# Kernel tuning notes

Measured on AMD Instinct MI355X. Metric: run time of the kernel, lower is better.

The kernel has to match this reference:

```python
import jax, jax.numpy as jnp
import numpy as np

N = 100000   # nodes
E = 1600000  # edges (avg degree 16)
H = 8        # heads
C = 64       # per-head channels
G = 64       # graphs in batch
IN = 3       # input channels
OUT = 10     # classes
NEG_SLOPE = 0.2  # PyG GATConv default


def setup_inputs() -> dict:
    key = jax.random.key(0)
    ks = jax.random.split(key, 16)
    s = 0.1
    return {
        "x": jax.random.normal(ks[0], (N, IN), jnp.float32),
        "edge_index": jax.random.randint(ks[1], (2, E), 0, N),
        "batch": jnp.sort(jax.random.randint(ks[2], (N,), 0, G)),
        "W1": jax.random.normal(ks[3], (IN, H * C), jnp.float32) * s,
        "a1s": jax.random.normal(ks[4], (H, C), jnp.float32) * s,
        "a1d": jax.random.normal(ks[5], (H, C), jnp.float32) * s,
        "b1": jnp.zeros((H * C,), jnp.float32),
        "W2": jax.random.normal(ks[6], (H * C, H * C), jnp.float32) * s,
        "a2s": jax.random.normal(ks[7], (H, C), jnp.float32) * s,
        "a2d": jax.random.normal(ks[8], (H, C), jnp.float32) * s,
        "b2": jnp.zeros((H * C,), jnp.float32),
        "Wc": jax.random.normal(ks[9], (H * C, OUT), jnp.float32) * s,
        "bc": jnp.zeros((OUT,), jnp.float32),
    }


def _gat_layer(x, W, a_s, a_d, b, src, dst, n):
    # h: [N, H, C] per-head projected features
    h = (x @ W).reshape(n, H, C)
    # per-node attention logits per head
    al_s = jnp.einsum('nhc,hc->nh', h, a_s)
    al_d = jnp.einsum('nhc,hc->nh', h, a_d)
    # per-edge raw scores, [E', H]
    e = jax.nn.leaky_relu(al_s[src] + al_d[dst], NEG_SLOPE)
    # segment softmax over incoming edges of each destination node
    m = jax.ops.segment_max(e, dst, num_segments=n)
    ex = jnp.exp(e - m[dst])
    den = jax.ops.segment_sum(ex, dst, num_segments=n)
    alpha = ex / den[dst]  # [E', H]
    # weighted scatter-aggregate of source messages
    out = jax.ops.segment_sum(alpha[:, :, None] * h[src], dst, num_segments=n)
    return out.reshape(n, H * C) + b


def reference(x, edge_index, batch, W1, a1s, a1d, b1, W2, a2s, a2d, b2, Wc, bc):
    n = x.shape[0]
    ar = jnp.arange(n)
    # PyG GATConv adds self-loops by default
    src = jnp.concatenate([edge_index[0], ar])
    dst = jnp.concatenate([edge_index[1], ar])

    x1 = jax.nn.elu(_gat_layer(x, W1, a1s, a1d, b1, src, dst, n))
    x2 = jax.nn.elu(_gat_layer(x1, W2, a2s, a2d, b2, src, dst, n))

    # global mean pool over graphs
    sums = jax.ops.segment_sum(x2, batch, num_segments=G)
    cnt = jax.ops.segment_sum(jnp.ones((n, 1), x2.dtype), batch, num_segments=G)
    pooled = sums / jnp.maximum(cnt, 1.0)
    return pooled @ Wc + bc
```

## Files before the change

kernel.cpp:

```cpp
#include <hip/hip_runtime.h>
#include <math.h>

#define N_NODES 100000
#define N_EDGES 1600000
#define EP (N_EDGES + N_NODES)
#define NH 8
#define NC 64
#define NG 64
#define HC 512
#define SCAN_BLOCKS ((N_NODES + 255) / 256)
#define NPART 32
#define BPSTR 80

typedef unsigned short bf16_t;
typedef unsigned char fp8_t;
typedef __attribute__((ext_vector_type(8))) short short8;
typedef __attribute__((ext_vector_type(4))) float floatx4;
typedef __attribute__((ext_vector_type(2))) float floatx2;

__device__ inline bf16_t f2bf(float f) {
    union { float f; unsigned int i; } x;
    x.f = f;
    unsigned int b = x.i;
    return (bf16_t)((b + 0x7fffu + ((b >> 16) & 1u)) >> 16);
}
__device__ inline fp8_t f2fp8(float f) {
    int v = __builtin_amdgcn_cvt_pk_fp8_f32(f, f, 0, false);
    return (fp8_t)v;
}

__device__ inline void ldsload16(const void* g, void* l) {
    __builtin_amdgcn_global_load_lds(
        (const __attribute__((address_space(1))) unsigned int*)g,
        (__attribute__((address_space(3))) unsigned int*)l, 16, 0, 0);
}

#define NBW2T (HC * HC / 256)
__global__ void k_prepw2t(const float* __restrict__ W1, const float* __restrict__ a1s,
                          const float* __restrict__ a1d, float* __restrict__ wprep,
                          const float* __restrict__ W2, bf16_t* __restrict__ W2T) {
    if (blockIdx.x == NBW2T) {
        int t = threadIdx.x;
        if (t < 48) {
            int isD = t >= 24;
            int tt = t % 24;
            int h = tt / 3, k = tt % 3;
            const float* a = isD ? a1d : a1s;
            float s = 0.f;
            for (int c = 0; c < 64; c++) s += W1[k * HC + h * 64 + c] * a[h * 64 + c];
            wprep[t] = s;
        }
        return;
    }
    int i = blockIdx.x * 256 + threadIdx.x;
    int n = i >> 9, kp = i & 511;
    int k = (kp & 7) * 64 + (kp >> 3);
    W2T[i] = f2bf(W2[k * HC + n]);
}

__global__ void k_deg(const int* __restrict__ ei, int* __restrict__ deg) {
    int i = blockIdx.x * 256 + threadIdx.x;
    if (i >= EP) return;
    int d = (i < N_EDGES) ? ei[N_EDGES + i] : (i - N_EDGES);
    atomicAdd(&deg[d], 1);
}

__global__ void k_scan1(const int* __restrict__ deg, int* __restrict__ rowptr, int* __restrict__ part) {
    __shared__ int s[256];
    int t = threadIdx.x, i = blockIdx.x * 256 + t;
    int v = (i < N_NODES) ? deg[i] : 0;
    s[t] = v;
    __syncthreads();
    for (int off = 1; off < 256; off <<= 1) {
        int u = (t >= off) ? s[t - off] : 0;
        __syncthreads();
        s[t] += u;
        __syncthreads();
    }
    if (i < N_NODES) rowptr[i] = s[t] - v;
    if (t == 255) part[blockIdx.x] = s[t];
}

__global__ void k_scan2(int* __restrict__ part, int* __restrict__ rowptr, int* __restrict__ gstart) {
    __shared__ int s[512];
    int t = threadIdx.x;
    int v = (t < SCAN_BLOCKS) ? part[t] : 0;
    s[t] = v;
    __syncthreads();
    for (int off = 1; off < 512; off <<= 1) {
        int u = (t >= off) ? s[t - off] : 0;
        __syncthreads();
        s[t] += u;
        __syncthreads();
    }
    part[t] = s[t] - v;
    if (t == 0) rowptr[N_NODES] = EP;
    if (t <= NG) gstart[t] = N_NODES;
}

__global__ void k_scan3(const int* __restrict__ part, int* __restrict__ rowptr,
                        int* __restrict__ cursor, const float* __restrict__ x,
                        float* __restrict__ xp, const int* __restrict__ batch,
                        int* __restrict__ gstart) {
    int i = blockIdx.x * 256 + threadIdx.x;
    if (i < N_NODES) {
        int v = rowptr[i] + part[blockIdx.x];
        rowptr[i] = v;
        cursor[i] = v;
        xp[i * 4 + 0] = x[i * 3 + 0];
        xp[i * 4 + 1] = x[i * 3 + 1];
        xp[i * 4 + 2] = x[i * 3 + 2];
        xp[i * 4 + 3] = 0.f;
        int b = batch[i];
        if (i == 0) {
            for (int g = 0; g <= b; g++) gstart[g] = 0;
        } else {
            int bp = batch[i - 1];
            if (b != bp)
                for (int g = bp + 1; g <= b; g++) gstart[g] = i;
        }
    }
}

__global__ void k_scatter(const int* __restrict__ ei, int* __restrict__ cursor, int* __restrict__ csr) {
    int i = blockIdx.x * 256 + threadIdx.x;
    if (i >= EP) return;
    int s, d;
    if (i < N_EDGES) { s = ei[i]; d = ei[N_EDGES + i]; }
    else { s = i - N_EDGES; d = s; }
    int pos = atomicAdd(&cursor[d], 1);
    csr[pos] = s;
}

__global__ __launch_bounds__(256) void k_layer1(
    const float* __restrict__ xp, const int* __restrict__ rowptr, const int* __restrict__ csr,
    const float* __restrict__ W1, const float* __restrict__ wprep, const float* __restrict__ b1,
    bf16_t* __restrict__ x1p) {
    __shared__ float w1s[1536];
    __shared__ float wp[48];
    int tid = threadIdx.x;
    for (int i = tid; i < 1536; i += 256) w1s[i] = W1[i];
    if (tid < 48) wp[tid] = wprep[tid];
    __syncthreads();
    int lane = tid & 63, wave = tid >> 6;
    int half = lane >> 5, l32 = lane & 31;
    int dst = blockIdx.x * 8 + wave * 2 + half;
    int rs = rowptr[dst], re = rowptr[dst + 1];
    float4 xd = *(const float4*)&xp[dst * 4];
    float ald[NH];
#pragma unroll
    for (int h = 0; h < NH; h++)
        ald[h] = xd.x * wp[24 + h * 3] + xd.y * wp[24 + h * 3 + 1] + xd.z * wp[24 + h * 3 + 2];
    float den[NH], c0[NH], c1[NH], c2[NH];
#pragma unroll
    for (int h = 0; h < NH; h++) { den[h] = 0.f; c0[h] = 0.f; c1[h] = 0.f; c2[h] = 0.f; }
    for (int base = rs; base < re; base += 32) {
        int e = base + l32;
        if (e < re) {
            int s = csr[e];
            float4 sv = *(const float4*)&xp[s * 4];
#pragma unroll
            for (int h = 0; h < NH; h++) {
                float ev = sv.x * wp[h * 3] + sv.y * wp[h * 3 + 1] + sv.z * wp[h * 3 + 2] + ald[h];
                ev = fmaxf(ev, 0.2f * ev);
                float w = __expf(ev);
                den[h] += w;
                c0[h] += w * sv.x;
                c1[h] += w * sv.y;
                c2[h] += w * sv.z;
            }
        }
    }
#pragma unroll
    for (int h = 0; h < NH; h++) {
#pragma unroll
        for (int off = 1; off < 32; off <<= 1) {
            den[h] += __shfl_xor(den[h], off, 64);
            c0[h] += __shfl_xor(c0[h], off, 64);
            c1[h] += __shfl_xor(c1[h], off, 64);
            c2[h] += __shfl_xor(c2[h], off, 64);
        }
    }
    bf16_t vbA[NH], vbB[NH];
#pragma unroll
    for (int h = 0; h < NH; h++) {
        int colA = h * 64 + l32;
        float vA = c0[h] * w1s[colA] + c1[h] * w1s[512 + colA] + c2[h] * w1s[1024 + colA];
        vA = vA / den[h] + b1[colA];
        vA = vA > 0.f ? vA : (__expf(vA) - 1.f);
        vbA[h] = f2bf(vA);
        int colB = colA + 32;
        float vB = c0[h] * w1s[colB] + c1[h] * w1s[512 + colB] + c2[h] * w1s[1024 + colB];
        vB = vB / den[h] + b1[colB];
        vB = vB > 0.f ? vB : (__expf(vB) - 1.f);
        vbB[h] = f2bf(vB);
    }
    uint4 oA, oB;
    oA.x = (unsigned int)vbA[0] | ((unsigned int)vbA[1] << 16);
    oA.y = (unsigned int)vbA[2] | ((unsigned int)vbA[3] << 16);
    oA.z = (unsigned int)vbA[4] | ((unsigned int)vbA[5] << 16);
    oA.w = (unsigned int)vbA[6] | ((unsigned int)vbA[7] << 16);
    oB.x = (unsigned int)vbB[0] | ((unsigned int)vbB[1] << 16);
    oB.y = (unsigned int)vbB[2] | ((unsigned int)vbB[3] << 16);
    oB.z = (unsigned int)vbB[4] | ((unsigned int)vbB[5] << 16);
    oB.w = (unsigned int)vbB[6] | ((unsigned int)vbB[7] << 16);
    *(uint4*)&x1p[(size_t)dst * HC + l32 * 8] = oA;
    *(uint4*)&x1p[(size_t)dst * HC + (l32 + 32) * 8] = oB;
}

__global__ __launch_bounds__(256) void k_gemm2(const bf16_t* __restrict__ A,
                                               const bf16_t* __restrict__ BT,
                                               fp8_t* __restrict__ Out,
                                               int row_base, int nrows,
                                               const float* __restrict__ a2s,
                                               const float* __restrict__ a2d,
                                               float* __restrict__ al2s,
                                               float* __restrict__ al2d) {
    __shared__ short smem[16384];
    short* As = smem;
    short* Bs = smem + 8192;
    int tid = threadIdx.x;
    int lane = tid & 63, wave = tid >> 6;
    int wm = wave & 1, wn = wave >> 1;
    int lm = lane & 15, quad = lane >> 4;
    int gx = blockIdx.x, gy = blockIdx.y;
    int l8 = lane >> 3, lc8 = lane & 7;
    int sw = lc8 ^ l8;
    const bf16_t* ga[4];
    const bf16_t* gb[4];
    short* la[4];
    short* lb[4];
#pragma unroll
    for (int it = 0; it < 4; it++) {
        int ar = gy * 128 + wave * 32 + it * 8 + l8;
        int arc = (ar < nrows) ? ar : 0;
        ga[it] = A + (size_t)(row_base + arc) * HC + sw * 8;
        gb[it] = BT + (size_t)(gx * 128 + wave * 32 + it * 8 + l8) * HC + sw * 8;
        la[it] = As + (wave * 32 + it * 8) * 64;
        lb[it] = Bs + (wave * 32 + it * 8) * 64;
    }

    floatx4 acc[4][4];
#pragma unroll
    for (int mi = 0; mi < 4; mi++)
#pragma unroll
        for (int ni = 0; ni < 4; ni++) acc[mi][ni] = (floatx4){0.f, 0.f, 0.f, 0.f};

    int lmw = lm & 7;
    for (int k0 = 0; k0 < HC; k0 += 64) {
        __syncthreads();
#pragma unroll
        for (int it = 0; it < 4; it++) ldsload16(ga[it] + k0, la[it]);
#pragma unroll
        for (int it = 0; it < 4; it++) ldsload16(gb[it] + k0, lb[it]);
        __syncthreads();
        short8 af[4][2], bf[4][2];
#pragma unroll
        for (int mi = 0; mi < 4; mi++)
#pragma unroll
            for (int kk = 0; kk < 2; kk++) {
                int pos = (kk * 4 + quad) ^ lmw;
                af[mi][kk] = *(const short8*)&As[(wm * 64 + mi * 16 + lm) * 64 + pos * 8];
            }
#pragma unroll
        for (int ni = 0; ni < 4; ni++)
#pragma unroll
            for (int kk = 0; kk < 2; kk++) {
                int pos = (kk * 4 + quad) ^ lmw;
                bf[ni][kk] = *(const short8*)&Bs[(wn * 64 + ni * 16 + lm) * 64 + pos * 8];
            }
#pragma unroll
        for (int mi = 0; mi < 4; mi++)
#pragma unroll
            for (int ni = 0; ni < 4; ni++) {
                acc[mi][ni] = __builtin_amdgcn_mfma_f32_16x16x32_bf16(af[mi][0], bf[ni][0], acc[mi][ni], 0, 0, 0);
                acc[mi][ni] = __builtin_amdgcn_mfma_f32_16x16x32_bf16(af[mi][1], bf[ni][1], acc[mi][ni], 0, 0, 0);
            }
    }
    int head = gx * 2 + wn;
    float a2sv[4], a2dv[4];
#pragma unroll
    for (int ni = 0; ni < 4; ni++) {
        int col = gx * 128 + wn * 64 + ni * 16 + lm;
        a2sv[ni] = a2s[col];
        a2dv[ni] = a2d[col];
    }
#pragma unroll
    for (int mi = 0; mi < 4; mi++) {
#pragma unroll
        for (int rg = 0; rg < 4; rg++) {
            int lrow = gy * 128 + wm * 64 + mi * 16 + quad * 4 + rg;
            float ps = 0.f, pd = 0.f;
#pragma unroll
            for (int ni = 0; ni < 4; ni++) {
                float v = acc[mi][ni][rg];
                ps += v * a2sv[ni];
                pd += v * a2dv[ni];
            }
#pragma unroll
            for (int off = 1; off < 16; off <<= 1) {
                ps += __shfl_xor(ps, off, 64);
                pd += __shfl_xor(pd, off, 64);
            }
            if (lrow < nrows && lm == 0) {
                int ar = row_base + lrow;
                al2s[ar * NH + head] = ps;
                al2d[ar * NH + head] = pd;
            }
        }
    }
    __syncthreads();
    unsigned char* bpatch = (unsigned char*)smem + wave * (32 * BPSTR);
#pragma unroll
    for (int p = 0; p < 2; p++) {
#pragma unroll
        for (int mih = 0; mih < 2; mih++) {
            int mi = p * 2 + mih;
#pragma unroll
            for (int ni = 0; ni < 4; ni++)
#pragma unroll
                for (int rg = 0; rg < 4; rg++) {
                    int rl = mih * 16 + quad * 4 + rg;
                    bpatch[rl * BPSTR + ni * 16 + lm] = f2fp8(acc[mi][ni][rg]);
                }
        }
#pragma unroll
        for (int it = 0; it < 2; it++) {
            int idx = it * 64 + lane;
            int rl = idx >> 2, c16 = idx & 3;
            uint4 v = *(uint4*)&bpatch[rl * BPSTR + c16 * 16];
            int lrow = gy * 128 + wm * 64 + p * 32 + rl;
            if (lrow < nrows)
                *(uint4*)&Out[(size_t)lrow * HC + wn * 64 + gx * 128 + c16 * 16] = v;
        }
        __syncthreads();
    }
}

__global__ __launch_bounds__(64) void k_layer2pool(
    const fp8_t* __restrict__ h2lo, const fp8_t* __restrict__ h2hi, int srows,
    const float* __restrict__ al2s, const float* __restrict__ al2d,
    const int* __restrict__ rowptr, const int* __restrict__ csr, const float* __restrict__ b2,
    const int* __restrict__ batch, float* __restrict__ poolpart) {
    __shared__ float wlds[512];
    __shared__ int slds[64];
    int lane = threadIdx.x;
    int hme = lane >> 3;
    int dst = blockIdx.x;
    int rs = rowptr[dst], re = rowptr[dst + 1];
    float4 d0 = *(const float4*)&al2d[dst * NH];
    float4 d1 = *(const float4*)&al2d[dst * NH + 4];
    float ald[NH] = {d0.x, d0.y, d0.z, d0.w, d1.x, d1.y, d1.z, d1.w};
    float den[NH], acc[8];
#pragma unroll
    for (int h = 0; h < NH; h++) den[h] = 0.f;
#pragma unroll
    for (int q = 0; q < 8; q++) acc[q] = 0.f;
    for (int base = rs; base < re; base += 64) {
        int e = base + lane;
        int cl = re - base; if (cl > 64) cl = 64;
        float w[NH];
        int s = 0;
        if (e < re) {
            s = csr[e];
            float4 p0 = *(const float4*)&al2s[s * NH];
            float4 p1 = *(const float4*)&al2s[s * NH + 4];
            float als[NH] = {p0.x, p0.y, p0.z, p0.w, p1.x, p1.y, p1.z, p1.w};
#pragma unroll
            for (int h = 0; h < NH; h++) {
                float ev = als[h] + ald[h];
                ev = fmaxf(ev, 0.2f * ev);
                w[h] = __expf(ev);
                den[h] += w[h];
            }
        } else {
#pragma unroll
            for (int h = 0; h < NH; h++) w[h] = 0.f;
        }
        slds[lane] = s;
        *(float4*)&wlds[lane * 8] = make_float4(w[0], w[1], w[2], w[3]);
        *(float4*)&wlds[lane * 8 + 4] = make_float4(w[4], w[5], w[6], w[7]);
        int j = 0;
        for (; j + 3 < cl; j += 4) {
            int s0 = slds[j + 0], s1 = slds[j + 1];
            int s2 = slds[j + 2], s3 = slds[j + 3];
            float w0 = wlds[(j + 0) * 8 + hme];
            float w1 = wlds[(j + 1) * 8 + hme];
            float w2 = wlds[(j + 2) * 8 + hme];
            float w3 = wlds[(j + 3) * 8 + hme];
            const fp8_t* b0 = (s0 < srows) ? (h2lo + (size_t)s0 * HC) : (h2hi + (size_t)(s0 - srows) * HC);
            const fp8_t* b1p = (s1 < srows) ? (h2lo + (size_t)s1 * HC) : (h2hi + (size_t)(s1 - srows) * HC);
            const fp8_t* b2p = (s2 < srows) ? (h2lo + (size_t)s2 * HC) : (h2hi + (size_t)(s2 - srows) * HC);
            const fp8_t* b3p = (s3 < srows) ? (h2lo + (size_t)s3 * HC) : (h2hi + (size_t)(s3 - srows) * HC);
            uint2 v0 = *(const uint2*)&b0[lane * 8];
            uint2 v1 = *(const uint2*)&b1p[lane * 8];
            uint2 v2 = *(const uint2*)&b2p[lane * 8];
            uint2 v3 = *(const uint2*)&b3p[lane * 8];
            floatx2 c;
            c = __builtin_amdgcn_cvt_pk_f32_fp8(v0.x, false); acc[0] += w0 * c.x; acc[1] += w0 * c.y;
            c = __builtin_amdgcn_cvt_pk_f32_fp8(v0.x, true);  acc[2] += w0 * c.x; acc[3] += w0 * c.y;
            c = __builtin_amdgcn_cvt_pk_f32_fp8(v0.y, false); acc[4] += w0 * c.x; acc[5] += w0 * c.y;
            c = __builtin_amdgcn_cvt_pk_f32_fp8(v0.y, true);  acc[6] += w0 * c.x; acc[7] += w0 * c.y;
            c = __builtin_amdgcn_cvt_pk_f32_fp8(v1.x, false); acc[0] += w1 * c.x; acc[1] += w1 * c.y;
            c = __builtin_amdgcn_cvt_pk_f32_fp8(v1.x, true);  acc[2] += w1 * c.x; acc[3] += w1 * c.y;
            c = __builtin_amdgcn_cvt_pk_f32_fp8(v1.y, false); acc[4] += w1 * c.x; acc[5] += w1 * c.y;
            c = __builtin_amdgcn_cvt_pk_f32_fp8(v1.y, true);  acc[6] += w1 * c.x; acc[7] += w1 * c.y;
            c = __builtin_amdgcn_cvt_pk_f32_fp8(v2.x, false); acc[0] += w2 * c.x; acc[1] += w2 * c.y;
            c = __builtin_amdgcn_cvt_pk_f32_fp8(v2.x, true);  acc[2] += w2 * c.x; acc[3] += w2 * c.y;
            c = __builtin_amdgcn_cvt_pk_f32_fp8(v2.y, false); acc[4] += w2 * c.x; acc[5] += w2 * c.y;
            c = __builtin_amdgcn_cvt_pk_f32_fp8(v2.y, true);  acc[6] += w2 * c.x; acc[7] += w2 * c.y;
            c = __builtin_amdgcn_cvt_pk_f32_fp8(v3.x, false); acc[0] += w3 * c.x; acc[1] += w3 * c.y;
            c = __builtin_amdgcn_cvt_pk_f32_fp8(v3.x, true);  acc[2] += w3 * c.x; acc[3] += w3 * c.y;
            c = __builtin_amdgcn_cvt_pk_f32_fp8(v3.y, false); acc[4] += w3 * c.x; acc[5] += w3 * c.y;
            c = __builtin_amdgcn_cvt_pk_f32_fp8(v3.y, true);  acc[6] += w3 * c.x; acc[7] += w3 * c.y;
        }
        for (; j < cl; j++) {
            int sA = slds[j];
            float wA = wlds[j * 8 + hme];
            const fp8_t* bA = (sA < srows) ? (h2lo + (size_t)sA * HC) : (h2hi + (size_t)(sA - srows) * HC);
            uint2 vA = *(const uint2*)&bA[lane * 8];
            floatx2 c;
            c = __builtin_amdgcn_cvt_pk_f32_fp8(vA.x, false); acc[0] += wA * c.x; acc[1] += wA * c.y;
            c = __builtin_amdgcn_cvt_pk_f32_fp8(vA.x, true);  acc[2] += wA * c.x; acc[3] += wA * c.y;
            c = __builtin_amdgcn_cvt_pk_f32_fp8(vA.y, false); acc[4] += wA * c.x; acc[5] += wA * c.y;
            c = __builtin_amdgcn_cvt_pk_f32_fp8(vA.y, true);  acc[6] += wA * c.x; acc[7] += wA * c.y;
        }
    }
#pragma unroll
    for (int h = 0; h < NH; h++)
#pragma unroll
        for (int off = 1; off < 64; off <<= 1) den[h] += __shfl_xor(den[h], off, 64);
    float dd = den[0];
#pragma unroll
    for (int h = 1; h < NH; h++) dd = (hme == h) ? den[h] : dd;
    float dinv = 1.0f / dd;
    float4 ba = *(const float4*)&b2[lane * 8];
    float4 bb = *(const float4*)&b2[lane * 8 + 4];
    float bv[8] = {ba.x, ba.y, ba.z, ba.w, bb.x, bb.y, bb.z, bb.w};
#pragma unroll
    for (int q = 0; q < 8; q++) {
        float v = acc[q] * dinv + bv[q];
        v = v > 0.f ? v : (__expf(v) - 1.f);
        wlds[lane * 8 + q] = v;
    }
    int g = batch[dst];
    float* pp = poolpart + ((size_t)(blockIdx.x & (NPART - 1)) * NG + g) * HC;
#pragma unroll
    for (int h = 0; h < NH; h++)
        atomicAdd(&pp[h * 64 + lane], wlds[h * 64 + lane]);
}

__global__ __launch_bounds__(256) void k_poolcls(const float* __restrict__ poolpart,
                                                 const int* __restrict__ gstart,
                                                 const float* __restrict__ Wc,
                                                 const float* __restrict__ bc,
                                                 float* __restrict__ out) {
    __shared__ float pl[512];
    int g = blockIdx.x, t = threadIdx.x;
    for (int c = t; c < HC; c += 256) {
        float s = 0.f;
        for (int p = 0; p < NPART; p++) s += poolpart[(size_t)p * NG * HC + g * HC + c];
        pl[c] = s;
    }
    __syncthreads();
    if (t < 10) {
        float cnt = fmaxf((float)(gstart[g + 1] - gstart[g]), 1.0f);
        float acc = 0.f;
        for (int k = 0; k < HC; k++) acc += pl[k] * Wc[k * 10 + t];
        out[g * 10 + t] = acc / cnt + bc[t];
    }
}

extern "C" void kernel_launch(void* const* d_in, const int* in_sizes, int n_in,
                              void* d_out, int out_size, void* d_ws, size_t ws_size,
                              hipStream_t stream) {
    const float* x   = (const float*)d_in[0];
    const int*   ei  = (const int*)d_in[1];
    const int*   bat = (const int*)d_in[2];
    const float* W1  = (const float*)d_in[3];
    const float* a1s = (const float*)d_in[4];
    const float* a1d = (const float*)d_in[5];
    const float* b1  = (const float*)d_in[6];
    const float* W2  = (const float*)d_in[7];
    const float* a2s = (const float*)d_in[8];
    const float* a2d = (const float*)d_in[9];
    const float* b2  = (const float*)d_in[10];
    const float* Wc  = (const float*)d_in[11];
    const float* bc  = (const float*)d_in[12];
    float* out = (float*)d_out;

    char* ws = (char*)d_ws;
    size_t off = 0;
    auto alloc = [&](size_t bytes) {
        size_t o = off;
        off += (bytes + 255) & ~(size_t)255;
        return o;
    };
    float*  wprep    = (float*)(ws + alloc(48 * 4));
    int*    rowptr   = (int*)(ws + alloc((size_t)(N_NODES + 1) * 4));
    int*    deg      = (int*)(ws + alloc((size_t)N_NODES * 4));
    int*    cursor   = (int*)(ws + alloc((size_t)N_NODES * 4));
    int*    part     = (int*)(ws + alloc(512 * 4));
    int*    gstart   = (int*)(ws + alloc(65 * 4));
    float*  xp       = (float*)(ws + alloc((size_t)N_NODES * 4 * 4));
    int*    csr      = (int*)(ws + alloc((size_t)EP * 4));
    bf16_t* x1b      = (bf16_t*)(ws + alloc((size_t)N_NODES * HC * 2));
    float*  al2s     = (float*)(ws + alloc((size_t)N_NODES * NH * 4));
    float*  al2d     = (float*)(ws + alloc((size_t)N_NODES * NH * 4));
    float*  poolpart = (float*)(ws + alloc((size_t)NPART * NG * HC * 4));
    bf16_t* W2T = (bf16_t*)deg;

    size_t rem = (ws_size > off) ? ws_size - off : 0;
    int nslices, srows;
    if (rem >= (size_t)N_NODES * HC)      { nslices = 1;  srows = N_NODES; }
    else if (rem >= (size_t)50000 * HC)   { nslices = 2;  srows = 50000; }
    else if (rem >= (size_t)25000 * HC)   { nslices = 4;  srows = 25000; }
    else if (rem >= (size_t)12500 * HC)   { nslices = 8;  srows = 12500; }
    else                                  { nslices = 16; srows = 6250; }
    fp8_t* T = (fp8_t*)(ws + alloc((size_t)srows * HC));
    fp8_t* h2hi = (fp8_t*)x1b;

    hipMemsetAsync(deg, 0, (size_t)N_NODES * 4, stream);
    hipMemsetAsync(poolpart, 0, (size_t)NPART * NG * HC * 4, stream);

    k_deg<<<(EP + 255) / 256, 256, 0, stream>>>(ei, deg);
    k_scan1<<<SCAN_BLOCKS, 256, 0, stream>>>(deg, rowptr, part);
    k_scan2<<<1, 512, 0, stream>>>(part, rowptr, gstart);
    k_scan3<<<SCAN_BLOCKS, 256, 0, stream>>>(part, rowptr, cursor, x, xp, bat, gstart);
    k_scatter<<<(EP + 255) / 256, 256, 0, stream>>>(ei, cursor, csr);
    k_prepw2t<<<NBW2T + 1, 256, 0, stream>>>(W1, a1s, a1d, wprep, W2, W2T);
    k_layer1<<<N_NODES / 8, 256, 0, stream>>>(xp, rowptr, csr, W1, wprep, b1, x1b);
    for (int s = 0; s < nslices; s++) {
        fp8_t* outp = (s == 0) ? T : (h2hi + (size_t)(s - 1) * srows * HC);
        k_gemm2<<<dim3(4, (srows + 127) / 128), 256, 0, stream>>>(
            x1b, W2T, outp, s * srows, srows, a2s, a2d, al2s, al2d);
    }
    k_layer2pool<<<N_NODES, 64, 0, stream>>>(T, h2hi, srows, al2s, al2d,
                                             rowptr, csr, b2, bat, poolpart);
    k_poolcls<<<NG, 256, 0, stream>>>(poolpart, gstart, Wc, bc, out);
}
```

Baseline: 718.0 us.

## Store layer-1 node inputs as bf16 and run layer-1 with one-wave blocks

The padded node input array is now stored in bf16 (8 bytes per node) instead of fp32 (16 bytes), which halves the bytes fetched by the random per-edge gathers in layer 1. Layer 1 is also relaunched with 64-thread blocks, each handling two destination nodes, instead of 256-thread blocks handling eight, and W1 is staged into shared memory with float4 loads. Each block now loads the whole 6 KB W1 tile for only two nodes, so W1 staging traffic per node rises. Rounding inputs to bf16 also adds precision error to the attention logits.

```diff
diff --git a/kernel.cpp b/kernel.cpp
--- a/kernel.cpp
+++ b/kernel.cpp
@@ -18,6 +18,11 @@
 typedef __attribute__((ext_vector_type(4))) float floatx4;
 typedef __attribute__((ext_vector_type(2))) float floatx2;
 
+__device__ inline float bf2f(bf16_t u) {
+    union { unsigned int i; float f; } x;
+    x.i = (unsigned int)u << 16;
+    return x.f;
+}
 __device__ inline bf16_t f2bf(float f) {
     union { float f; unsigned int i; } x;
     x.f = f;
@@ -100,17 +105,19 @@
 
 __global__ void k_scan3(const int* __restrict__ part, int* __restrict__ rowptr,
                         int* __restrict__ cursor, const float* __restrict__ x,
-                        float* __restrict__ xp, const int* __restrict__ batch,
+                        bf16_t* __restrict__ xb, const int* __restrict__ batch,
                         int* __restrict__ gstart) {
     int i = blockIdx.x * 256 + threadIdx.x;
     if (i < N_NODES) {
         int v = rowptr[i] + part[blockIdx.x];
         rowptr[i] = v;
         cursor[i] = v;
-        xp[i * 4 + 0] = x[i * 3 + 0];
-        xp[i * 4 + 1] = x[i * 3 + 1];
-        xp[i * 4 + 2] = x[i * 3 + 2];
-        xp[i * 4 + 3] = 0.f;
+        ushort4 p;
+        p.x = f2bf(x[i * 3 + 0]);
+        p.y = f2bf(x[i * 3 + 1]);
+        p.z = f2bf(x[i * 3 + 2]);
+        p.w = 0;
+        *(ushort4*)&xb[i * 4] = p;
         int b = batch[i];
         if (i == 0) {
             for (int g = 0; g <= b; g++) gstart[g] = 0;
@@ -132,25 +139,27 @@
     csr[pos] = s;
 }
 
-__global__ __launch_bounds__(256) void k_layer1(
-    const float* __restrict__ xp, const int* __restrict__ rowptr, const int* __restrict__ csr,
+__global__ __launch_bounds__(64) void k_layer1(
+    const bf16_t* __restrict__ xb, const int* __restrict__ rowptr, const int* __restrict__ csr,
     const float* __restrict__ W1, const float* __restrict__ wprep, const float* __restrict__ b1,
     bf16_t* __restrict__ x1p) {
     __shared__ float w1s[1536];
     __shared__ float wp[48];
-    int tid = threadIdx.x;
-    for (int i = tid; i < 1536; i += 256) w1s[i] = W1[i];
-    if (tid < 48) wp[tid] = wprep[tid];
+    int lane = threadIdx.x;
+#pragma unroll
+    for (int q = 0; q < 6; q++)
+        *(float4*)&w1s[(q * 64 + lane) * 4] = *(const float4*)&W1[(q * 64 + lane) * 4];
+    if (lane < 48) wp[lane] = wprep[lane];
     __syncthreads();
-    int lane = tid & 63, wave = tid >> 6;
     int half = lane >> 5, l32 = lane & 31;
-    int dst = blockIdx.x * 8 + wave * 2 + half;
+    int dst = blockIdx.x * 2 + half;
     int rs = rowptr[dst], re = rowptr[dst + 1];
-    float4 xd = *(const float4*)&xp[dst * 4];
+    ushort4 xd4 = *(const ushort4*)&xb[dst * 4];
+    float xdx = bf2f(xd4.x), xdy = bf2f(xd4.y), xdz = bf2f(xd4.z);
     float ald[NH];
 #pragma unroll
     for (int h = 0; h < NH; h++)
-        ald[h] = xd.x * wp[24 + h * 3] + xd.y * wp[24 + h * 3 + 1] + xd.z * wp[24 + h * 3 + 2];
+        ald[h] = xdx * wp[24 + h * 3] + xdy * wp[24 + h * 3 + 1] + xdz * wp[24 + h * 3 + 2];
     float den[NH], c0[NH], c1[NH], c2[NH];
 #pragma unroll
     for (int h = 0; h < NH; h++) { den[h] = 0.f; c0[h] = 0.f; c1[h] = 0.f; c2[h] = 0.f; }
@@ -158,16 +167,17 @@
         int e = base + l32;
         if (e < re) {
             int s = csr[e];
-            float4 sv = *(const float4*)&xp[s * 4];
+            ushort4 sv4 = *(const ushort4*)&xb[s * 4];
+            float svx = bf2f(sv4.x), svy = bf2f(sv4.y), svz = bf2f(sv4.z);
 #pragma unroll
             for (int h = 0; h < NH; h++) {
-                float ev = sv.x * wp[h * 3] + sv.y * wp[h * 3 + 1] + sv.z * wp[h * 3 + 2] + ald[h];
+                float ev = svx * wp[h * 3] + svy * wp[h * 3 + 1] + svz * wp[h * 3 + 2] + ald[h];
                 ev = fmaxf(ev, 0.2f * ev);
                 float w = __expf(ev);
                 den[h] += w;
-                c0[h] += w * sv.x;
-                c1[h] += w * sv.y;
-                c2[h] += w * sv.z;
+                c0[h] += w * svx;
+                c1[h] += w * svy;
+                c2[h] += w * svz;
             }
         }
     }
@@ -502,7 +512,7 @@
     int*    cursor   = (int*)(ws + alloc((size_t)N_NODES * 4));
     int*    part     = (int*)(ws + alloc(512 * 4));
     int*    gstart   = (int*)(ws + alloc(65 * 4));
-    float*  xp       = (float*)(ws + alloc((size_t)N_NODES * 4 * 4));
+    bf16_t* xb       = (bf16_t*)(ws + alloc((size_t)N_NODES * 4 * 2));
     int*    csr      = (int*)(ws + alloc((size_t)EP * 4));
     bf16_t* x1b      = (bf16_t*)(ws + alloc((size_t)N_NODES * HC * 2));
     float*  al2s     = (float*)(ws + alloc((size_t)N_NODES * NH * 4));
@@ -526,10 +536,10 @@
     k_deg<<<(EP + 255) / 256, 256, 0, stream>>>(ei, deg);
     k_scan1<<<SCAN_BLOCKS, 256, 0, stream>>>(deg, rowptr, part);
     k_scan2<<<1, 512, 0, stream>>>(part, rowptr, gstart);
-    k_scan3<<<SCAN_BLOCKS, 256, 0, stream>>>(part, rowptr, cursor, x, xp, bat, gstart);
+    k_scan3<<<SCAN_BLOCKS, 256, 0, stream>>>(part, rowptr, cursor, x, xb, bat, gstart);
     k_scatter<<<(EP + 255) / 256, 256, 0, stream>>>(ei, cursor, csr);
     k_prepw2t<<<NBW2T + 1, 256, 0, stream>>>(W1, a1s, a1d, wprep, W2, W2T);
-    k_layer1<<<N_NODES / 8, 256, 0, stream>>>(xp, rowptr, csr, W1, wprep, b1, x1b);
+    k_layer1<<<N_NODES / 2, 64, 0, stream>>>(xb, rowptr, csr, W1, wprep, b1, x1b);
     for (int s = 0; s < nslices; s++) {
         fp8_t* outp = (s == 0) ? T : (h2hi + (size_t)(s - 1) * srows * HC);
         k_gemm2<<<dim3(4, (srows + 127) / 128), 256, 0, stream>>>(
```

Measured after the change: 715.6 us. No clear change (-0.3%).
